# Kernel tuning notes

Hardware: AMD Instinct MI355X
Metric: run time of the kernel (lower is better)

The kernel has to match this reference:

```python
import jax, jax.numpy as jnp
import numpy as np

EPS2D = 0.3          # gsplat classic-mode 2D blur added to covariance diagonal
SZ2 = 0.001 ** 2     # sigma_z^2 from the fixed z-scale 0.001
ALPHA_MAX = 0.999    # gsplat alpha clamp


def setup_inputs() -> dict:
    key = jax.random.key(0)
    k0, k1, k2, k3, k4 = jax.random.split(key, 5)
    B, N, H, W = 2, 768, 160, 160
    means = jax.random.uniform(k0, (B, N, 2), jnp.float32, 0.0, float(W))      # pixel coords
    scales = jax.random.uniform(k1, (B, N, 2), jnp.float32, 1.0, 8.0)          # pixel scales
    rotations = jax.random.normal(k2, (B, N, 1), jnp.float32)                  # radians
    colors = jax.random.uniform(k3, (B, N, 3), jnp.float32)                    # RGB [0,1]
    opacities = jax.random.uniform(k4, (B, N, 1), jnp.float32)                 # [0,1]
    return {"means": means, "scales": scales, "rotations": rotations,
            "colors": colors, "opacities": opacities, "H": H, "W": W}


def reference(means, scales, rotations, colors, opacities, H, W):
    B, N, _ = means.shape
    dt = means.dtype
    # quat (cos t/2, 0, 0, sin t/2) == rotation about z by t; cov3d = R diag(sx^2,sy^2,sz^2) R^T
    theta = rotations[..., 0]
    c, s = jnp.cos(theta), jnp.sin(theta)
    sx2, sy2 = scales[..., 0] ** 2, scales[..., 1] ** 2
    a = c * c * sx2 + s * s * sy2            # xy-block of 3D covariance
    b = c * s * (sx2 - sy2)
    d = s * s * sx2 + c * c * sy2
    mx, my = means[..., 0], means[..., 1]
    # viewmat=I, K=I, z=1 -> projected mean = (x, y); Jacobian J = [[1,0,-x],[0,1,-y]]
    # cov2d = J cov3d J^T + eps2d * I  (z-block contributes sz^2 * [x,y] outer [x,y])
    cov_xx = a + SZ2 * mx * mx + EPS2D
    cov_xy = b + SZ2 * mx * my
    cov_yy = d + SZ2 * my * my + EPS2D
    det = cov_xx * cov_yy - cov_xy * cov_xy
    ca, cb, cc = cov_yy / det, -cov_xy / det, cov_xx / det   # conic (inverse cov)

    px = jnp.arange(W, dtype=dt) + 0.5       # pixel centers
    py = jnp.arange(H, dtype=dt) + 0.5
    gx, gy = jnp.meshgrid(px, py)            # (H, W)
    dx = gx.reshape(-1)[None, :, None] - mx[:, None, :]      # (B, HW, N)
    dy = gy.reshape(-1)[None, :, None] - my[:, None, :]
    q = (ca[:, None, :] * dx * dx
         + 2.0 * cb[:, None, :] * dx * dy
         + cc[:, None, :] * dy * dy)
    alpha = jnp.minimum(opacities[:, None, :, 0] * jnp.exp(-0.5 * q), ALPHA_MAX)

    # front-to-back compositing (all depths == 1 -> stable input order)
    log1m = jnp.log1p(-alpha)                                 # (B, HW, N)
    T = jnp.exp(jnp.cumsum(log1m, axis=-1) - log1m)           # exclusive cumprod of (1-alpha)
    w = alpha * T                                             # per-gaussian pixel weight
    img = jnp.einsum('bpn,bnc->bpc', w, colors)               # (B, HW, 3)
    img = img.reshape(B, H, W, 3).transpose(0, 3, 1, 2)       # (B, 3, H, W)
    return jnp.clip(img, 0.0, 1.0)
```

## Files before the change

### kernel.cpp

```cpp
#include <hip/hip_runtime.h>
#include <hip/hip_fp16.h>
#include <string.h>

#define BATCH   2
#define NG      768
#define H_      160
#define W_      160
#define NPIX    (H_ * W_)
#define NCHUNK  8
#define CHUNK   (NG / NCHUNK)
#define TILE    8
#define TPD     (W_ / TILE)
#define NTILE   (TPD * TPD)
#define EPS2D_  0.3f
#define SZ2_    1.0e-6f
#define ALPHA_MAX_ 0.999f
#define KEXP    (-0.7213475204444817f)
#define LN_CULL_EPS (-13.815511f)


__global__ __launch_bounds__(256)
void gr_precompute(const float* __restrict__ means,
                   const float* __restrict__ scales,
                   const float* __restrict__ rots,
                   const float* __restrict__ colors,
                   const float* __restrict__ opac,
                   float4* __restrict__ cull, float4* __restrict__ pay, int total) {
    int i = blockIdx.x * blockDim.x + threadIdx.x;
    if (i >= total) return;
    float theta = rots[i];
    float c = cosf(theta), s = sinf(theta);
    float sx = scales[2*i], sy = scales[2*i+1];
    float sx2 = sx*sx, sy2 = sy*sy;
    float a  = c*c*sx2 + s*s*sy2;
    float bb = c*s*(sx2 - sy2);
    float d  = s*s*sx2 + c*c*sy2;
    float mx = means[2*i], my = means[2*i+1];
    float cxx = a + SZ2_*mx*mx + EPS2D_;
    float cxy = bb + SZ2_*mx*my;
    float cyy = d + SZ2_*my*my + EPS2D_;
    float det = cxx*cyy - cxy*cxy;
    float inv = 1.0f / det;
    float ca  =  cyy * inv;
    float cb2 = -cxy * inv;
    float cc  =  cxx * inv;
    float op  = opac[i];

    float k2 = 2.0f * (logf(op) - LN_CULL_EPS);
    k2 = fmaxf(k2, 0.0f);
    float kk = sqrtf(k2);
    float ex = kk * sqrtf(cxx);
    float ey = kk * sqrtf(cyy);
    cull[i] = make_float4(mx, my, ex, ey);

    float A = KEXP * ca;
    float B = KEXP * 2.0f * cb2;
    float C = KEXP * cc;
    float D = KEXP * (-2.0f * ca * mx - 2.0f * cb2 * my);
    float E = KEXP * (-2.0f * cc * my - 2.0f * cb2 * mx);
    float F = KEXP * (ca*mx*mx + 2.0f*cb2*mx*my + cc*my*my) + log2f(op);
    float cr = colors[3*i], cg = colors[3*i+1], cb = colors[3*i+2];
    __half2 h2 = __floats2half2_rn(cr, cg);
    float rg; memcpy(&rg, &h2, 4);
    pay[2*i]   = make_float4(A, B, C, D);
    pay[2*i+1] = make_float4(E, F, rg, cb);
}

__global__ __launch_bounds__(256)
void gr_render(const float4* __restrict__ cull, const float4* __restrict__ pay,
               float4* __restrict__ part) {
    __shared__ float4 lds[4][CHUNK * 2];
    int tid  = threadIdx.x;
    int wave = tid >> 6;
    int lane = tid & 63;
    int tile = blockIdx.x;
    int chunk = blockIdx.y * 4 + wave;
    int b    = blockIdx.z;
    int tx = tile % TPD, ty = tile / TPD;
    int pxi = tx * TILE + (lane & 7);
    int pyi = ty * TILE + (lane >> 3);
    float px = (float)pxi + 0.5f;
    float py = (float)pyi + 0.5f;
    float cxm = (float)(tx * TILE) + 0.5f * TILE;
    float cym = (float)(ty * TILE) + 0.5f * TILE;
    const float RH = 0.5f * TILE;

    int base = b * NG + chunk * CHUNK;
    int cnt = 0;

    {
        float4 cu = cull[base + lane];
        bool keep = (fabsf(cu.x - cxm) <= cu.z + RH) &&
                    (fabsf(cu.y - cym) <= cu.w + RH);
        unsigned long long m = __ballot(keep);
        unsigned pre = __builtin_amdgcn_mbcnt_hi((unsigned)(m >> 32),
                        __builtin_amdgcn_mbcnt_lo((unsigned)m, 0u));
        if (keep) {
            int gi = base + lane;
            lds[wave][2*pre]     = pay[2*gi];
            lds[wave][2*pre + 1] = pay[2*gi + 1];
        }
        cnt = (int)__popcll(m);
    }
    {
        bool valid = lane < (CHUNK - 64);
        int gi = base + 64 + (valid ? lane : 0);
        float4 cu = cull[gi];
        bool keep = valid &&
                    (fabsf(cu.x - cxm) <= cu.z + RH) &&
                    (fabsf(cu.y - cym) <= cu.w + RH);
        unsigned long long m = __ballot(keep);
        unsigned pre = __builtin_amdgcn_mbcnt_hi((unsigned)(m >> 32),
                        __builtin_amdgcn_mbcnt_lo((unsigned)m, 0u));
        if (keep) {
            int slot = cnt + (int)pre;
            lds[wave][2*slot]     = pay[2*gi];
            lds[wave][2*slot + 1] = pay[2*gi + 1];
        }
        cnt += (int)__popcll(m);
    }

    float r = 0.f, g = 0.f, bl = 0.f, T = 1.f;
    float x2 = px*px, xy = px*py, y2 = py*py;
    for (int i = 0; i < cnt; ++i) {
        float4 av = lds[wave][2*i];
        float4 ev = lds[wave][2*i + 1];
        float q = fmaf(av.x, x2,
                  fmaf(av.y, xy,
                  fmaf(av.z, y2,
                  fmaf(av.w, px,
                  fmaf(ev.x, py, ev.y)))));
        float al = fminf(__builtin_exp2f(q), ALPHA_MAX_);
        float w  = T * al;
        __half2 h2; memcpy(&h2, &ev.z, 4);
        float2 rg = __half22float2(h2);
        r  = fmaf(w, rg.x, r);
        g  = fmaf(w, rg.y, g);
        bl = fmaf(w, ev.w, bl);
        T -= w;
        if (((i & 7) == 7) && __all(T < 1.0e-4f)) break;
    }
    part[(chunk * BATCH + b) * NPIX + pyi * W_ + pxi] = make_float4(r, g, bl, T);
}

__global__ __launch_bounds__(256)
void gr_combine(const float4* __restrict__ part, float* __restrict__ out) {
    int idx = blockIdx.x * 256 + threadIdx.x;
    if (idx >= BATCH * NPIX) return;
    int b = idx / NPIX;
    int p = idx - b * NPIX;
    float4 o = part[((NCHUNK-1) * BATCH + b) * NPIX + p];
    float r = o.x, gg = o.y, bb = o.z;
    #pragma unroll
    for (int i = NCHUNK-2; i >= 0; --i) {
        float4 oi = part[(i * BATCH + b) * NPIX + p];
        r  = fmaf(oi.w, r,  oi.x);
        gg = fmaf(oi.w, gg, oi.y);
        bb = fmaf(oi.w, bb, oi.z);
    }
    r  = fminf(fmaxf(r , 0.f), 1.f);
    gg = fminf(fmaxf(gg, 0.f), 1.f);
    bb = fminf(fmaxf(bb, 0.f), 1.f);
    out[(b * 3 + 0) * NPIX + p] = r;
    out[(b * 3 + 1) * NPIX + p] = gg;
    out[(b * 3 + 2) * NPIX + p] = bb;
}

extern "C" void kernel_launch(void* const* d_in, const int* in_sizes, int n_in,
                              void* d_out, int out_size, void* d_ws, size_t ws_size,
                              hipStream_t stream) {
    const float* means  = (const float*)d_in[0];
    const float* scales = (const float*)d_in[1];
    const float* rots   = (const float*)d_in[2];
    const float* colors = (const float*)d_in[3];
    const float* opac   = (const float*)d_in[4];
    float* out = (float*)d_out;

    int total = BATCH * NG;
    float4* cullA = (float4*)d_ws;
    float4* pay   = cullA + total;
    float4* part  = pay + 2 * total;

    gr_precompute<<<(total + 255) / 256, 256, 0, stream>>>(
        means, scales, rots, colors, opac, cullA, pay, total);

    dim3 rgrid(NTILE, NCHUNK / 4, BATCH);
    gr_render<<<rgrid, 256, 0, stream>>>(cullA, pay, part);

    gr_combine<<<(BATCH * NPIX + 255) / 256, 256, 0, stream>>>(part, out);
}
```

Before: 77.80 us.

## Fuse chunk combine into render kernel via LDS partial compositing

Each wave now processes two consecutive gaussian chunks sequentially, with early termination across them. The four wave partials are combined in shared memory inside the render block and written straight to the output. This drops the global partial buffer, its write-and-reread traffic, and the separate combine kernel launch. The cost is half as many render blocks, so less parallelism, and each wave does serial work over two chunks.

Result: faster. 73.65 us (-5.3%).

```diff
diff --git a/kernel.cpp b/kernel.cpp
--- a/kernel.cpp
+++ b/kernel.cpp
@@ -68,14 +68,14 @@
 
 __global__ __launch_bounds__(256)
 void gr_render(const float4* __restrict__ cull, const float4* __restrict__ pay,
-               float4* __restrict__ part) {
-    __shared__ float4 lds[4][CHUNK * 2];
+               float* __restrict__ out) {
+    __shared__ float4 stage[4][CHUNK * 2];
+    __shared__ float4 partl[4][64];
     int tid  = threadIdx.x;
     int wave = tid >> 6;
     int lane = tid & 63;
     int tile = blockIdx.x;
-    int chunk = blockIdx.y * 4 + wave;
-    int b    = blockIdx.z;
+    int b    = blockIdx.y;
     int tx = tile % TPD, ty = tile / TPD;
     int pxi = tx * TILE + (lane & 7);
     int pyi = ty * TILE + (lane >> 3);
@@ -84,86 +84,86 @@
     float cxm = (float)(tx * TILE) + 0.5f * TILE;
     float cym = (float)(ty * TILE) + 0.5f * TILE;
     const float RH = 0.5f * TILE;
+    float x2 = px*px, xy = px*py, y2 = py*py;
 
-    int base = b * NG + chunk * CHUNK;
-    int cnt = 0;
+    float R = 0.f, G = 0.f, B = 0.f, T = 1.f;
 
-    {
-        float4 cu = cull[base + lane];
-        bool keep = (fabsf(cu.x - cxm) <= cu.z + RH) &&
-                    (fabsf(cu.y - cym) <= cu.w + RH);
-        unsigned long long m = __ballot(keep);
-        unsigned pre = __builtin_amdgcn_mbcnt_hi((unsigned)(m >> 32),
-                        __builtin_amdgcn_mbcnt_lo((unsigned)m, 0u));
-        if (keep) {
-            int gi = base + lane;
-            lds[wave][2*pre]     = pay[2*gi];
-            lds[wave][2*pre + 1] = pay[2*gi + 1];
+    #pragma unroll
+    for (int cc = 0; cc < 2; ++cc) {
+        int chunk = wave * 2 + cc;
+        int base  = b * NG + chunk * CHUNK;
+        int cnt = 0;
+
+        {
+            float4 cu = cull[base + lane];
+            bool keep = (fabsf(cu.x - cxm) <= cu.z + RH) &&
+                        (fabsf(cu.y - cym) <= cu.w + RH);
+            unsigned long long m = __ballot(keep);
+            unsigned pre = __builtin_amdgcn_mbcnt_hi((unsigned)(m >> 32),
+                            __builtin_amdgcn_mbcnt_lo((unsigned)m, 0u));
+            if (keep) {
+                int gi = base + lane;
+                stage[wave][2*pre]     = pay[2*gi];
+                stage[wave][2*pre + 1] = pay[2*gi + 1];
+            }
+            cnt = (int)__popcll(m);
         }
-        cnt = (int)__popcll(m);
-    }
-    {
-        bool valid = lane < (CHUNK - 64);
-        int gi = base + 64 + (valid ? lane : 0);
-        float4 cu = cull[gi];
-        bool keep = valid &&
-                    (fabsf(cu.x - cxm) <= cu.z + RH) &&
-                    (fabsf(cu.y - cym) <= cu.w + RH);
-        unsigned long long m = __ballot(keep);
-        unsigned pre = __builtin_amdgcn_mbcnt_hi((unsigned)(m >> 32),
-                        __builtin_amdgcn_mbcnt_lo((unsigned)m, 0u));
-        if (keep) {
-            int slot = cnt + (int)pre;
-            lds[wave][2*slot]     = pay[2*gi];
-            lds[wave][2*slot + 1] = pay[2*gi + 1];
+        {
+            bool valid = lane < (CHUNK - 64);
+            int gi = base + 64 + (valid ? lane : 0);
+            float4 cu = cull[gi];
+            bool keep = valid &&
+                        (fabsf(cu.x - cxm) <= cu.z + RH) &&
+                        (fabsf(cu.y - cym) <= cu.w + RH);
+            unsigned long long m = __ballot(keep);
+            unsigned pre = __builtin_amdgcn_mbcnt_hi((unsigned)(m >> 32),
+                            __builtin_amdgcn_mbcnt_lo((unsigned)m, 0u));
+            if (keep) {
+                int slot = cnt + (int)pre;
+                stage[wave][2*slot]     = pay[2*gi];
+                stage[wave][2*slot + 1] = pay[2*gi + 1];
+            }
+            cnt += (int)__popcll(m);
         }
-        cnt += (int)__popcll(m);
+
+        for (int i = 0; i < cnt; ++i) {
+            float4 av = stage[wave][2*i];
+            float4 ev = stage[wave][2*i + 1];
+            float q = fmaf(av.x, x2,
+                      fmaf(av.y, xy,
+                      fmaf(av.z, y2,
+                      fmaf(av.w, px,
+                      fmaf(ev.x, py, ev.y)))));
+            float al = fminf(__builtin_exp2f(q), ALPHA_MAX_);
+            float w  = T * al;
+            __half2 h2; memcpy(&h2, &ev.z, 4);
+            float2 rg = __half22float2(h2);
+            R  = fmaf(w, rg.x, R);
+            G  = fmaf(w, rg.y, G);
+            B  = fmaf(w, ev.w, B);
+            T -= w;
+            if (((i & 7) == 7) && __all(T < 1.0e-4f)) break;
+        }
+        if (__all(T < 1.0e-4f)) break;
     }
 
-    float r = 0.f, g = 0.f, bl = 0.f, T = 1.f;
-    float x2 = px*px, xy = px*py, y2 = py*py;
-    for (int i = 0; i < cnt; ++i) {
-        float4 av = lds[wave][2*i];
-        float4 ev = lds[wave][2*i + 1];
-        float q = fmaf(av.x, x2,
-                  fmaf(av.y, xy,
-                  fmaf(av.z, y2,
-                  fmaf(av.w, px,
-                  fmaf(ev.x, py, ev.y)))));
-        float al = fminf(__builtin_exp2f(q), ALPHA_MAX_);
-        float w  = T * al;
-        __half2 h2; memcpy(&h2, &ev.z, 4);
-        float2 rg = __half22float2(h2);
-        r  = fmaf(w, rg.x, r);
-        g  = fmaf(w, rg.y, g);
-        bl = fmaf(w, ev.w, bl);
-        T -= w;
-        if (((i & 7) == 7) && __all(T < 1.0e-4f)) break;
-    }
-    part[(chunk * BATCH + b) * NPIX + pyi * W_ + pxi] = make_float4(r, g, bl, T);
-}
+    partl[wave][lane] = make_float4(R, G, B, T);
+    __syncthreads();
 
-__global__ __launch_bounds__(256)
-void gr_combine(const float4* __restrict__ part, float* __restrict__ out) {
-    int idx = blockIdx.x * 256 + threadIdx.x;
-    if (idx >= BATCH * NPIX) return;
-    int b = idx / NPIX;
-    int p = idx - b * NPIX;
-    float4 o = part[((NCHUNK-1) * BATCH + b) * NPIX + p];
-    float r = o.x, gg = o.y, bb = o.z;
+    float4 o = partl[3][lane];
+    float r = o.x, g = o.y, bb = o.z;
     #pragma unroll
-    for (int i = NCHUNK-2; i >= 0; --i) {
-        float4 oi = part[(i * BATCH + b) * NPIX + p];
+    for (int i = 2; i >= 0; --i) {
+        float4 oi = partl[i][lane];
         r  = fmaf(oi.w, r,  oi.x);
-        gg = fmaf(oi.w, gg, oi.y);
+        g  = fmaf(oi.w, g,  oi.y);
         bb = fmaf(oi.w, bb, oi.z);
     }
-    r  = fminf(fmaxf(r , 0.f), 1.f);
-    gg = fminf(fmaxf(gg, 0.f), 1.f);
-    bb = fminf(fmaxf(bb, 0.f), 1.f);
-    out[(b * 3 + 0) * NPIX + p] = r;
-    out[(b * 3 + 1) * NPIX + p] = gg;
-    out[(b * 3 + 2) * NPIX + p] = bb;
+    if (wave < 3) {
+        float v = (wave == 0) ? r : (wave == 1) ? g : bb;
+        v = fminf(fmaxf(v, 0.f), 1.f);
+        out[(b * 3 + wave) * NPIX + pyi * W_ + pxi] = v;
+    }
 }
 
 extern "C" void kernel_launch(void* const* d_in, const int* in_sizes, int n_in,
@@ -179,13 +179,10 @@
     int total = BATCH * NG;
     float4* cullA = (float4*)d_ws;
     float4* pay   = cullA + total;
-    float4* part  = pay + 2 * total;
 
     gr_precompute<<<(total + 255) / 256, 256, 0, stream>>>(
         means, scales, rots, colors, opac, cullA, pay, total);
 
-    dim3 rgrid(NTILE, NCHUNK / 4, BATCH);
-    gr_render<<<rgrid, 256, 0, stream>>>(cullA, pay, part);
-
-    gr_combine<<<(BATCH * NPIX + 255) / 256, 256, 0, stream>>>(part, out);
+    dim3 rgrid(NTILE, BATCH);
+    gr_render<<<rgrid, 256, 0, stream>>>(cullA, pay, out);
 }
```
